# Kernel optimization log

Measured on AMD Instinct MI355X. Metric: run time of the kernel, lower is better.

Reference implementation:

```python
import jax, jax.numpy as jnp
import numpy as np

MC_SAMPLES = 32  # k neighbors
BIG = 1e8


def _swish(x):
    return x * jax.nn.sigmoid(x)


def setup_inputs() -> dict:
    key = jax.random.key(0)
    ks = jax.random.split(key, 8)
    bs, n, d, c = 8, 1024, 3, 64
    cmco_ci, hid = 16, 32
    abq_pairs = jax.random.normal(ks[0], (bs, n, n, d), dtype=jnp.float32)
    vals = jax.random.normal(ks[1], (bs, n, c), dtype=jnp.float32)
    mask = jnp.ones((bs, n), dtype=bool)
    s = 0.1
    return {
        "abq_pairs": abq_pairs,
        "vals": vals,
        "mask": mask,
        "W1": jax.random.normal(ks[2], (d, hid), dtype=jnp.float32) * s,
        "b1": jnp.zeros((hid,), jnp.float32),
        "W2": jax.random.normal(ks[3], (hid, hid), dtype=jnp.float32) * s,
        "b2": jnp.zeros((hid,), jnp.float32),
        "W3": jax.random.normal(ks[4], (hid, cmco_ci), dtype=jnp.float32) * s,
        "b3": jnp.zeros((cmco_ci,), jnp.float32),
        "Wl": jax.random.normal(ks[5], (c * cmco_ci, c), dtype=jnp.float32) * s,
        "bl": jnp.zeros((c,), jnp.float32),
    }


def reference(abq_pairs, vals, mask, W1, b1, W2, b2, W3, b3, Wl, bl):
    bs, n, _, d = abq_pairs.shape
    c = vals.shape[-1]
    k = min(MC_SAMPLES, n)

    # --- extract_neighborhood (knn branch, ds_frac=1 so queries = all points) ---
    # Trivial group distance = norm over last dim of abq pairs: (bs,n,n)
    dists = jnp.linalg.norm(abq_pairs, axis=-1)
    dists = jnp.where(mask[:, None, :], dists, BIG)
    _, nbhd_idx = jax.lax.top_k(-dists, k)  # smallest-k -> (bs, n, k)

    # gather neighbor pairwise embeddings: (bs, n, k, d)
    nbhd_abq = jnp.take_along_axis(abq_pairs, nbhd_idx[..., None], axis=2)
    # gather neighbor values and mask per batch: (bs, n, k, c), (bs, n, k)
    nbhd_vals = jax.vmap(lambda v, i: v[i])(vals, nbhd_idx)
    nbhd_mask = jax.vmap(lambda m, i: m[i])(mask, nbhd_idx) & mask[:, :, None]

    h = _swish(nbhd_abq @ W1 + b1)
    h = _swish(h @ W2 + b2)
    penult_kernel_weights = _swish(h @ W3 + b3)  # (bs, n, k, 16)

    # --- masked weighted aggregation (generalized PointConv trick) ---
    mW = jnp.where(nbhd_mask[..., None], penult_kernel_weights, 0.0)
    mV = jnp.where(nbhd_mask[..., None], nbhd_vals, 0.0)
    # vals^T @ weights -> (bs, n, c, 16) -> (bs, n, c*16)
    partial = jnp.einsum("bmkc,bmkp->bmcp", mV, mW).reshape(bs, n, -1)
    convolved = partial @ Wl + bl  # (bs, n, c)

    # zero out invalid query points
    return jnp.where(mask[..., None], convolved, 0.0)
```

## Files before the change

### kernel.cpp

```cpp
#include <hip/hip_runtime.h>
#include <math.h>


#define NPTS 1024
#define KNB  32
#define CCH  64
#define HID  32
#define PCH  16

#define OFF_PACK    196608
#define PACKN       1808
#define OFF_WLB_U16 262144

typedef __bf16        bf16x8 __attribute__((ext_vector_type(8)));
typedef float         f32x4  __attribute__((ext_vector_type(4)));
typedef unsigned int  uint4v __attribute__((ext_vector_type(4)));

__device__ __forceinline__ float swishf(float x) {
    return x * __builtin_amdgcn_rcpf(1.0f + __expf(-x));
}

__device__ __forceinline__ unsigned bf16rne(float f) {
    unsigned u = __float_as_uint(f);
    return (u + 0x7fffu + ((u >> 16) & 1u)) >> 16;
}

__global__ __launch_bounds__(256) void lieconv_pack(
    const float* __restrict__ W1, const float* __restrict__ b1,
    const float* __restrict__ W2, const float* __restrict__ b2,
    const float* __restrict__ W3, const float* __restrict__ b3,
    const float* __restrict__ Wl, float* __restrict__ ws)
{
    const int tid = threadIdx.x;
    if (blockIdx.x == 0) {
        float* pack = ws + OFF_PACK;
        for (int idx = tid; idx < PACKN; idx += 256) {
            float v;
            if (idx < 128) {
                int i4 = idx >> 4, rem = idx & 15, r = rem >> 2, u = rem & 3;
                v = (r < 3) ? W1[r * 32 + i4 * 4 + u] : b1[i4 * 4 + u];
            } else if (idx < 1792) {
                int oi = idx - 128;
                int o = oi / 52, t = oi - o * 52;
                if (t < 32)       v = W2[t * 32 + o];
                else if (t < 48)  v = W3[o * 16 + (t - 32)];
                else if (t == 48) v = b2[o];
                else              v = 0.0f;
            } else {
                v = b3[idx - 1792];
            }
            pack[idx] = v;
        }
    } else {
        const int t   = (blockIdx.x - 1) * 256 + tid;
        const int g   = t >> 6, l = t & 63;
        const int k0  = (g >> 2) * 32 + ((l >> 4) << 3);
        const int col = ((g & 3) << 4) + (l & 15);
        unsigned us[8];
#pragma unroll
        for (int j = 0; j < 8; ++j)
            us[j] = bf16rne(Wl[(size_t)(k0 + j) * 64 + col]);
        uint4 pk;
        pk.x = us[0] | (us[1] << 16);
        pk.y = us[2] | (us[3] << 16);
        pk.z = us[4] | (us[5] << 16);
        pk.w = us[6] | (us[7] << 16);
        *(uint4*)((unsigned short*)ws + OFF_WLB_U16 + (size_t)t * 8) = pk;
    }
}

#define WVS 20

__global__ __launch_bounds__(256, 4) void lieconv_fused(
    const float* __restrict__ abq, const float* __restrict__ vals,
    const float* __restrict__ ws_ro, const float* __restrict__ bl,
    float* __restrict__ out)
{
    __shared__ __align__(16) float s_mem[10112];
    float* s_pack = s_mem;
    float* s_wv   = s_mem + 4096;
    char*  spb    = (char*)s_mem;
    float* s_nb   = s_mem + 9216;
    unsigned short* s_sel = (unsigned short*)(s_mem + 9984);

    const int tid  = threadIdx.x;
    const int lane = tid & 63;
    const int w    = tid >> 6;
    const size_t r0 = (size_t)blockIdx.x * 8;

#pragma unroll
    for (int u = 0; u < 8; ++u) {
        int idx = u * 256 + tid;
        if (idx < PACKN) s_pack[idx] = ws_ro[OFF_PACK + idx];
    }

    {
        int* s_cand = (int*)(s_mem + 4096) + w * 64;
        const unsigned long long lmask = (1ull << lane) - 1ull;
        for (int rr = 0; rr < 2; ++rr) {
            const int lr = w * 2 + rr;
            const float* __restrict__ rowp = abq + (r0 + lr) * (size_t)(NPTS * 3);

            float kf[16];
#pragma unroll
            for (int q = 0; q < 16; ++q) {
                int j = q * 64 + lane;
                float x = rowp[j * 3 + 0];
                float y = rowp[j * 3 + 1];
                float z = rowp[j * 3 + 2];
                kf[q] = fmaf(x, x, fmaf(y, y, z * z));
            }
            float kmax = kf[0];
#pragma unroll
            for (int q = 1; q < 16; ++q) kmax = fmaxf(kmax, kf[q]);
#pragma unroll
            for (int off = 32; off > 0; off >>= 1)
                kmax = fmaxf(kmax, __shfl_xor(kmax, off, 64));

            float lo = 0.0f, hi = kmax * 1.000001f + 1e-30f, T = hi;
            for (int it = 0; it < 28; ++it) {
                float mid = 0.5f * (lo + hi);
                int c = 0;
#pragma unroll
                for (int q = 0; q < 16; ++q)
                    c += __popcll(__ballot(kf[q] < mid));
                if (c < KNB)      lo = mid;
                else if (c > 40)  hi = mid;
                else { T = mid; break; }
                T = hi;
            }
            float Tcut = T * 1.000001f;

            int base = 0;
#pragma unroll
            for (int q = 0; q < 16; ++q) {
                bool p = kf[q] < Tcut;
                unsigned long long mk = __ballot(p);
                int pos = base + __popcll(mk & lmask);
                if (p && pos < 64) s_cand[pos] = q * 64 + lane;
                base += __popcll(mk);
            }
            int ncand = (base < 64) ? base : 64;

            unsigned long long ci = ~0ull;
            int ji = 0x7fffffff;
            double xd = 0.0, yd = 0.0, zd = 0.0;
            if (lane < ncand) {
                ji = s_cand[lane];
                xd = (double)rowp[ji * 3 + 0];
                yd = (double)rowp[ji * 3 + 1];
                zd = (double)rowp[ji * 3 + 2];
                double ki = (xd * xd + yd * yd) + zd * zd;
                ci = ((unsigned long long)__double_as_longlong(ki) & ~1023ull) | (unsigned)ji;
            }
            int rank = 0;
#pragma unroll
            for (int t = 0; t < 64; ++t) {
                unsigned long long ct = __shfl(ci, t, 64);
                rank += (ct < ci) ? 1 : 0;
            }
            bool selb = (lane < ncand) && (rank < KNB);
            unsigned long long mk = __ballot(selb);
            if (selb) {
                int pos = lr * KNB + __popcll(mk & lmask);
                s_sel[pos] = (unsigned short)ji;
                float* nbp = s_nb + pos * 3;
                nbp[0] = (float)xd;
                nbp[1] = (float)yd;
                nbp[2] = (float)zd;
            }
        }
    }
    __syncthreads();

    {
        float x = s_nb[tid * 3 + 0];
        float y = s_nb[tid * 3 + 1];
        float z = s_nb[tid * 3 + 2];

        const float4* __restrict__ w1p = (const float4*)s_pack;
        const float4* __restrict__ opk = (const float4*)s_pack + 32;
        const float4* __restrict__ b3q = (const float4*)(s_pack + 1792);

        float h1[32];
#pragma unroll
        for (int i4 = 0; i4 < 8; ++i4) {
            float4 qa = w1p[i4 * 4 + 0];
            float4 qb = w1p[i4 * 4 + 1];
            float4 qc = w1p[i4 * 4 + 2];
            float4 qd = w1p[i4 * 4 + 3];
            h1[i4 * 4 + 0] = swishf(fmaf(x, qa.x, fmaf(y, qb.x, fmaf(z, qc.x, qd.x))));
            h1[i4 * 4 + 1] = swishf(fmaf(x, qa.y, fmaf(y, qb.y, fmaf(z, qc.y, qd.y))));
            h1[i4 * 4 + 2] = swishf(fmaf(x, qa.z, fmaf(y, qb.z, fmaf(z, qc.z, qd.z))));
            h1[i4 * 4 + 3] = swishf(fmaf(x, qa.w, fmaf(y, qb.w, fmaf(z, qc.w, qd.w))));
        }

        float wv[16];
        {
            float4 q0 = b3q[0], q1 = b3q[1], q2 = b3q[2], q3 = b3q[3];
            wv[0]=q0.x; wv[1]=q0.y; wv[2]=q0.z; wv[3]=q0.w;
            wv[4]=q1.x; wv[5]=q1.y; wv[6]=q1.z; wv[7]=q1.w;
            wv[8]=q2.x; wv[9]=q2.y; wv[10]=q2.z; wv[11]=q2.w;
            wv[12]=q3.x; wv[13]=q3.y; wv[14]=q3.z; wv[15]=q3.w;
        }
#pragma unroll
        for (int o = 0; o < 32; ++o) {
            const float4* q = opk + o * 13;
            float acc = q[12].x;
#pragma unroll
            for (int n = 0; n < 8; ++n) {
                float4 qq = q[n];
                acc = fmaf(h1[n * 4 + 0], qq.x, acc);
                acc = fmaf(h1[n * 4 + 1], qq.y, acc);
                acc = fmaf(h1[n * 4 + 2], qq.z, acc);
                acc = fmaf(h1[n * 4 + 3], qq.w, acc);
            }
            float h2 = swishf(acc);
#pragma unroll
            for (int n = 0; n < 4; ++n) {
                float4 qq = q[8 + n];
                wv[n * 4 + 0] = fmaf(h2, qq.x, wv[n * 4 + 0]);
                wv[n * 4 + 1] = fmaf(h2, qq.y, wv[n * 4 + 1]);
                wv[n * 4 + 2] = fmaf(h2, qq.z, wv[n * 4 + 2]);
                wv[n * 4 + 3] = fmaf(h2, qq.w, wv[n * 4 + 3]);
            }
        }
        float* wo = &s_wv[tid * WVS];
#pragma unroll
        for (int n = 0; n < 4; ++n)
            *(float4*)&wo[n * 4] = make_float4(swishf(wv[n * 4 + 0]), swishf(wv[n * 4 + 1]),
                                               swishf(wv[n * 4 + 2]), swishf(wv[n * 4 + 3]));
    }
    __syncthreads();

    const int p4    = (lane & 3) * 4;
    const int cbase = lane >> 2;
#pragma unroll
    for (int rr = 0; rr < 2; ++rr) {
        const int lr = w * 2 + rr;
        const size_t R = r0 + lr;
        const float* __restrict__ valsb = vals + (R >> 10) * (size_t)(NPTS * CCH);

        int jj_l = (int)s_sel[lr * 32 + (lane & 31)];

        float acc[4][4];
#pragma unroll
        for (int it = 0; it < 4; ++it)
#pragma unroll
            for (int e = 0; e < 4; ++e) acc[it][e] = 0.0f;

#pragma unroll 8
        for (int kk = 0; kk < KNB; ++kk) {
            int jj = __shfl(jj_l, kk, 64);
            float4 wq = *(const float4*)&s_wv[(lr * 32 + kk) * WVS + p4];
            const float* vr = valsb + (size_t)jj * CCH + cbase;
#pragma unroll
            for (int it = 0; it < 4; ++it) {
                float v = vr[16 * it];
                acc[it][0] = fmaf(v, wq.x, acc[it][0]);
                acc[it][1] = fmaf(v, wq.y, acc[it][1]);
                acc[it][2] = fmaf(v, wq.z, acc[it][2]);
                acc[it][3] = fmaf(v, wq.w, acc[it][3]);
            }
        }
        const unsigned xr = (unsigned)((lr & 7) << 4);
#pragma unroll
        for (int it = 0; it < 4; ++it) {
            int c = cbase + 16 * it;
            unsigned kb  = (unsigned)(c * 32 + p4 * 2);
            unsigned off = (unsigned)(lr * 2048) + (kb ^ xr);
            uint2 pkv;
            pkv.x = bf16rne(acc[it][0]) | (bf16rne(acc[it][1]) << 16);
            pkv.y = bf16rne(acc[it][2]) | (bf16rne(acc[it][3]) << 16);
            *(uint2*)(spb + off) = pkv;
        }
    }
    __syncthreads();

    {
        const int arow = lane & 15;
        const int kgrp = lane >> 4;
        const bf16x8* __restrict__ wlb8 =
            (const bf16x8*)((const unsigned short*)ws_ro + OFF_WLB_U16) + (w * 64 + lane);

        uint4v zz = {0u, 0u, 0u, 0u};
        const bf16x8 a0 = __builtin_bit_cast(bf16x8, zz);
        f32x4 acc = {0.0f, 0.0f, 0.0f, 0.0f};

        const unsigned x     = (unsigned)((arow & 7) << 4);
        const unsigned abase = (unsigned)(arow * 2048) + ((unsigned)(kgrp * 16) ^ (x & 48u));
        const unsigned xl    = x & 64u;
#pragma unroll 8
        for (int s = 0; s < 32; ++s) {
            bf16x8 a = a0;
            if (arow < 8)
                a = *(const bf16x8*)(spb + (abase + (((unsigned)(s * 64)) ^ xl)));
            bf16x8 b = wlb8[(size_t)s * 256];
            acc = __builtin_amdgcn_mfma_f32_16x16x32_bf16(a, b, acc, 0, 0, 0);
        }
        if (kgrp < 2) {
            const int cc   = w * 16 + arow;
            const float bias = bl[cc];
#pragma unroll
            for (int r4 = 0; r4 < 4; ++r4)
                out[(r0 + kgrp * 4 + r4) * 64 + cc] = acc[r4] + bias;
        }
    }
}

extern "C" void kernel_launch(void* const* d_in, const int* in_sizes, int n_in,
                              void* d_out, int out_size, void* d_ws, size_t ws_size,
                              hipStream_t stream)
{
    const float* abq  = (const float*)d_in[0];
    const float* vals = (const float*)d_in[1];
    const float* W1 = (const float*)d_in[3];
    const float* b1 = (const float*)d_in[4];
    const float* W2 = (const float*)d_in[5];
    const float* b2 = (const float*)d_in[6];
    const float* W3 = (const float*)d_in[7];
    const float* b3 = (const float*)d_in[8];
    const float* Wl = (const float*)d_in[9];
    const float* bl = (const float*)d_in[10];
    float* out = (float*)d_out;

    float* ws = (float*)d_ws;

    hipLaunchKernelGGL(lieconv_pack, dim3(33), dim3(256), 0, stream,
                       W1, b1, W2, b2, W3, b3, Wl, ws);
    hipLaunchKernelGGL(lieconv_fused, dim3(1024), dim3(256), 0, stream,
                       abq, vals, ws, bl, out);
}
```

Measured before the change: 208.3 us.

## Speed up kNN selection with preset thresholds, float4 loads and bitonic sort

Per-row top-k selection now first tests three fixed squared-distance thresholds in a single pass. It falls back to a narrowed bisection only when none of them yields between 32 and 60 candidates. Row data is loaded as coalesced float4 vectors, with point indices remapped to match. The second row's load is issued before the first row is processed, to overlap memory latency. The 64-step shuffle rank count is replaced by a bitonic sort across the wave. The preset thresholds are tuned to the expected distance distribution, but the fallback keeps results correct for other inputs.

```diff
diff --git a/kernel.cpp b/kernel.cpp
--- a/kernel.cpp
+++ b/kernel.cpp
@@ -97,39 +97,58 @@
     {
         int* s_cand = (int*)(s_mem + 4096) + w * 64;
         const unsigned long long lmask = (1ull << lane) - 1ull;
-        for (int rr = 0; rr < 2; ++rr) {
-            const int lr = w * 2 + rr;
-            const float* __restrict__ rowp = abq + (r0 + lr) * (size_t)(NPTS * 3);
-
-            float kf[16];
+        const float T1 = 0.20f, T2 = 0.32f, T3 = 0.48f;
+
+        const float* __restrict__ rowp0 = abq + (r0 + w * 2 + 0) * (size_t)(NPTS * 3);
+        const float* __restrict__ rowp1 = abq + (r0 + w * 2 + 1) * (size_t)(NPTS * 3);
+
+        auto keys4 = [&](const float4& a, const float4& b, const float4& c, float* kk) {
+            kk[0] = fmaf(a.x, a.x, fmaf(a.y, a.y, a.z * a.z));
+            kk[1] = fmaf(a.w, a.w, fmaf(b.x, b.x, b.y * b.y));
+            kk[2] = fmaf(b.z, b.z, fmaf(b.w, b.w, c.x * c.x));
+            kk[3] = fmaf(c.y, c.y, fmaf(c.z, c.z, c.w * c.w));
+        };
+
+        auto prow = [&](const float* __restrict__ rowp, const float kf[16], int lr) {
+            int c1 = 0, c2 = 0, c3 = 0;
 #pragma unroll
             for (int q = 0; q < 16; ++q) {
-                int j = q * 64 + lane;
-                float x = rowp[j * 3 + 0];
-                float y = rowp[j * 3 + 1];
-                float z = rowp[j * 3 + 2];
-                kf[q] = fmaf(x, x, fmaf(y, y, z * z));
-            }
-            float kmax = kf[0];
-#pragma unroll
-            for (int q = 1; q < 16; ++q) kmax = fmaxf(kmax, kf[q]);
-#pragma unroll
-            for (int off = 32; off > 0; off >>= 1)
-                kmax = fmaxf(kmax, __shfl_xor(kmax, off, 64));
-
-            float lo = 0.0f, hi = kmax * 1.000001f + 1e-30f, T = hi;
-            for (int it = 0; it < 28; ++it) {
-                float mid = 0.5f * (lo + hi);
-                int c = 0;
-#pragma unroll
-                for (int q = 0; q < 16; ++q)
-                    c += __popcll(__ballot(kf[q] < mid));
-                if (c < KNB)      lo = mid;
-                else if (c > 40)  hi = mid;
-                else { T = mid; break; }
-                T = hi;
-            }
-            float Tcut = T * 1.000001f;
+                float kq = kf[q];
+                c1 += __popcll(__ballot(kq < T1));
+                c2 += __popcll(__ballot(kq < T2));
+                c3 += __popcll(__ballot(kq < T3));
+            }
+            float Tsel;
+            if (c1 >= 32 && c1 <= 60)      Tsel = T1;
+            else if (c2 >= 32 && c2 <= 60) Tsel = T2;
+            else if (c3 >= 32 && c3 <= 60) Tsel = T3;
+            else {
+                float kmax = kf[0];
+#pragma unroll
+                for (int q = 1; q < 16; ++q) kmax = fmaxf(kmax, kf[q]);
+#pragma unroll
+                for (int off = 32; off > 0; off >>= 1)
+                    kmax = fmaxf(kmax, __shfl_xor(kmax, off, 64));
+                float lo = (c3 < 32) ? T3 : (c2 < 32) ? T2 : (c1 < 32) ? T1 : 0.0f;
+                float hi = kmax * 1.000001f + 1e-30f;
+                if (c1 > 60)      hi = fminf(hi, T1);
+                else if (c2 > 60) hi = fminf(hi, T2);
+                else if (c3 > 60) hi = fminf(hi, T3);
+                if (lo >= hi) lo = 0.0f;
+                Tsel = hi;
+                for (int it = 0; it < 28; ++it) {
+                    float mid = 0.5f * (lo + hi);
+                    int c = 0;
+#pragma unroll
+                    for (int q = 0; q < 16; ++q)
+                        c += __popcll(__ballot(kf[q] < mid));
+                    if (c < 32)      lo = mid;
+                    else if (c > 60) hi = mid;
+                    else { Tsel = mid; break; }
+                    Tsel = hi;
+                }
+            }
+            float Tcut = Tsel * 1.000001f;
 
             int base = 0;
 #pragma unroll
@@ -137,39 +156,70 @@
                 bool p = kf[q] < Tcut;
                 unsigned long long mk = __ballot(p);
                 int pos = base + __popcll(mk & lmask);
-                if (p && pos < 64) s_cand[pos] = q * 64 + lane;
+                int j = (q >> 2) * 256 + lane * 4 + (q & 3);
+                if (p && pos < 64) s_cand[pos] = j;
                 base += __popcll(mk);
             }
             int ncand = (base < 64) ? base : 64;
 
             unsigned long long ci = ~0ull;
-            int ji = 0x7fffffff;
-            double xd = 0.0, yd = 0.0, zd = 0.0;
             if (lane < ncand) {
-                ji = s_cand[lane];
-                xd = (double)rowp[ji * 3 + 0];
-                yd = (double)rowp[ji * 3 + 1];
-                zd = (double)rowp[ji * 3 + 2];
-                double ki = (xd * xd + yd * yd) + zd * zd;
+                int ji = s_cand[lane];
+                double x = (double)rowp[ji * 3 + 0];
+                double y = (double)rowp[ji * 3 + 1];
+                double z = (double)rowp[ji * 3 + 2];
+                double ki = (x * x + y * y) + z * z;
                 ci = ((unsigned long long)__double_as_longlong(ki) & ~1023ull) | (unsigned)ji;
             }
-            int rank = 0;
-#pragma unroll
-            for (int t = 0; t < 64; ++t) {
-                unsigned long long ct = __shfl(ci, t, 64);
-                rank += (ct < ci) ? 1 : 0;
-            }
-            bool selb = (lane < ncand) && (rank < KNB);
-            unsigned long long mk = __ballot(selb);
-            if (selb) {
-                int pos = lr * KNB + __popcll(mk & lmask);
-                s_sel[pos] = (unsigned short)ji;
-                float* nbp = s_nb + pos * 3;
-                nbp[0] = (float)xd;
-                nbp[1] = (float)yd;
-                nbp[2] = (float)zd;
-            }
-        }
+#pragma unroll
+            for (int kk = 2; kk <= 64; kk <<= 1) {
+#pragma unroll
+                for (int j = kk >> 1; j > 0; j >>= 1) {
+                    unsigned long long o = __shfl_xor(ci, j, 64);
+                    bool takeMin = ((lane & kk) == 0) == ((lane & j) == 0);
+                    unsigned long long mn = (o < ci) ? o : ci;
+                    unsigned long long mx = (o < ci) ? ci : o;
+                    ci = takeMin ? mn : mx;
+                }
+            }
+            if (lane < KNB) {
+                int ji = (int)(ci & 1023ull);
+                s_sel[lr * 32 + lane] = (unsigned short)ji;
+                float* nbp = s_nb + (lr * 32 + lane) * 3;
+                nbp[0] = rowp[ji * 3 + 0];
+                nbp[1] = rowp[ji * 3 + 1];
+                nbp[2] = rowp[ji * 3 + 2];
+            }
+        };
+
+        const float4* __restrict__ rp40 = (const float4*)rowp0;
+        const float4* __restrict__ rp41 = (const float4*)rowp1;
+        float4 rawA[12];
+#pragma unroll
+        for (int pa = 0; pa < 4; ++pa)
+#pragma unroll
+            for (int t = 0; t < 3; ++t)
+                rawA[pa * 3 + t] = rp40[pa * 192 + lane * 3 + t];
+        float kfA[16];
+#pragma unroll
+        for (int pa = 0; pa < 4; ++pa)
+            keys4(rawA[pa * 3 + 0], rawA[pa * 3 + 1], rawA[pa * 3 + 2], &kfA[pa * 4]);
+
+        float4 rawB[12];
+#pragma unroll
+        for (int pa = 0; pa < 4; ++pa)
+#pragma unroll
+            for (int t = 0; t < 3; ++t)
+                rawB[pa * 3 + t] = rp41[pa * 192 + lane * 3 + t];
+
+        prow(rowp0, kfA, w * 2 + 0);
+
+        float kfB[16];
+#pragma unroll
+        for (int pa = 0; pa < 4; ++pa)
+            keys4(rawB[pa * 3 + 0], rawB[pa * 3 + 1], rawB[pa * 3 + 2], &kfB[pa * 4]);
+
+        prow(rowp1, kfB, w * 2 + 1);
     }
     __syncthreads();
 
```

Result: no change. 205.1 us (-1.5%).
